# Kernel tuning notes

Hardware: AMD Instinct MI355X
Metric: run time of the kernel (lower is better)

Reference implementation:

```python
import jax, jax.numpy as jnp
import numpy as np

BS, V, S, K = 4, 2048, 7, 10
CLASS_NUM, VEC_NUM, CAT = 6, 8, 16
OUT_HEAD = CLASS_NUM + VEC_NUM * 3  # 30
DIM_FUSE = 128 + 128 + 256 + 256 + 512 + 512 + 16  # 1808


def _normalize(x, axis):
    return x / jnp.maximum(jnp.linalg.norm(x, axis=axis, keepdims=True), 1e-12)


def knn_index(verts, k):
    # verts: (b, v, 3) -> (b, v, k) excluding self
    inner = jnp.einsum('bnd,bmd->bnm', verts, verts)
    sq = jnp.sum(verts * verts, axis=2)
    dist = sq[:, :, None] + sq[:, None, :] - 2.0 * inner
    _, idx = jax.lax.top_k(-dist, k + 1)
    return idx[:, :, 1:]


def nearest_index(target, source):
    # target: (b, v1, 3), source: (b, v2, 3) -> (b, v1)
    inner = jnp.einsum('bnd,bmd->bnm', target, source)
    d = jnp.sum(source * source, 2)[:, None, :] + jnp.sum(target * target, 2)[:, :, None] - 2.0 * inner
    return jnp.argmin(d, axis=-1)


def gather_nb(t, idx):
    # t: (b, v, d), idx: (b, v1, k) -> (b, v1, k, d)
    return jax.vmap(lambda tt, ii: tt[ii])(t, idx)


def gather1(t, idx):
    # t: (b, v, d), idx: (b, v1) -> (b, v1, d)
    return jax.vmap(lambda tt, ii: tt[ii])(t, idx)


def bn_train(x, g, b, eps=1e-5):
    # x: (b, v, c); BatchNorm1d training-mode over (batch, vertices)
    m = jnp.mean(x, axis=(0, 1), keepdims=True)
    v = jnp.var(x, axis=(0, 1), keepdims=True)
    return (x - m) * jax.lax.rsqrt(v + eps) * g + b


def conv_surface(nb_idx, verts, directions, s, kernel_num):
    nd = _normalize(gather_nb(verts, nb_idx) - verts[:, :, None, :], -1)  # (b,v,n,3)
    sd = _normalize(directions, 0)  # (3, s*k)
    theta = jax.nn.relu(jnp.einsum('bvnd,dk->bvnk', nd, sd))
    b_, v_, n_, _ = theta.shape
    theta = theta.reshape(b_, v_, n_, s, kernel_num)
    return jnp.sum(jnp.max(theta, axis=2), axis=2)  # (b, v, kernel_num)


def conv_layer(nb_idx, verts, fm, w, b, directions, s, out_ch):
    nd = _normalize(gather_nb(verts, nb_idx) - verts[:, :, None, :], -1)
    sd = _normalize(directions, 0)  # (3, s*out_ch)
    theta = jax.nn.relu(jnp.einsum('bvnd,dk->bvnk', nd, sd))  # (b,v,n,s*o)
    fo = jnp.einsum('bvc,ck->bvk', fm, w) + b  # (b, v, (s+1)*o)
    center = fo[..., :out_ch]
    supp = gather_nb(fo[..., out_ch:], nb_idx)  # (b,v,n,s*o)
    act = (theta * supp).reshape(theta.shape[0], theta.shape[1], theta.shape[2], s, out_ch)
    act = jnp.sum(jnp.max(act, axis=2), axis=2)  # (b, v, o)
    return center + act


def pool_layer(verts, fm, pooling_rate, nb_num):
    idx = knn_index(verts, nb_num)
    pooled = jnp.max(gather_nb(fm, idx), axis=2)
    pool_num = verts.shape[1] // pooling_rate
    # deterministic subsample (torch uses randperm; fixed arange for reproducibility)
    return verts[:, :pool_num], pooled[:, :pool_num]


def setup_inputs() -> dict:
    key = jax.random.key(0)
    ks = jax.random.split(key, 16)
    def rn(i, shape, scale=0.05):
        return jax.random.normal(ks[i], shape, dtype=jnp.float32) * scale
    z = lambda *s: jnp.zeros(s, jnp.float32)
    o = lambda *s: jnp.ones(s, jnp.float32)
    return {
        'vertices': jax.random.normal(ks[0], (BS, V, 3), dtype=jnp.float32),
        'onehot': jax.nn.one_hot(jax.random.randint(ks[1], (BS,), 0, CAT), CAT, dtype=jnp.float32),
        'dir0': rn(2, (3, S * 128)),
        'w1': rn(3, (128, (S + 1) * 128)), 'b1': z((S + 1) * 128), 'dir1': rn(4, (3, S * 128)),
        'w2': rn(5, (128, (S + 1) * 256)), 'b2': z((S + 1) * 256), 'dir2': rn(6, (3, S * 256)),
        'w3': rn(7, (256, (S + 1) * 256)), 'b3': z((S + 1) * 256), 'dir3': rn(8, (3, S * 256)),
        'w4': rn(9, (256, (S + 1) * 512)), 'b4': z((S + 1) * 512), 'dir4': rn(10, (3, S * 512)),
        'g_bn1': o(128), 'be_bn1': z(128),
        'g_bn2': o(256), 'be_bn2': z(256),
        'g_bn3': o(256), 'be_bn3': z(256),
        'wc1': rn(11, (512, DIM_FUSE)), 'bc1': z(512),
        'wc2': rn(12, (512, 512)), 'bc2': z(512),
        'wc3': rn(13, (OUT_HEAD, 512)), 'bc3': z(OUT_HEAD),
    }


def reference(vertices, onehot, dir0, w1, b1, dir1, w2, b2, dir2, w3, b3, dir3,
              w4, b4, dir4, g_bn1, be_bn1, g_bn2, be_bn2, g_bn3, be_bn3,
              wc1, bc1, wc2, bc2, wc3, bc3):
    bs, v_num, _ = vertices.shape
    nb = knn_index(vertices, K)
    fm0 = jax.nn.relu(conv_surface(nb, vertices, dir0, S, 128))
    fm1 = jax.nn.relu(bn_train(conv_layer(nb, vertices, fm0, w1, b1, dir1, S, 128), g_bn1, be_bn1))
    vp1, fp1 = pool_layer(vertices, fm1, 4, 4)
    nb1 = knn_index(vp1, min(K, vp1.shape[1] // 8))
    fm2 = jax.nn.relu(bn_train(conv_layer(nb1, vp1, fp1, w2, b2, dir2, S, 256), g_bn2, be_bn2))
    fm3 = jax.nn.relu(bn_train(conv_layer(nb1, vp1, fm2, w3, b3, dir3, S, 256), g_bn3, be_bn3))
    vp2, fp2 = pool_layer(vp1, fm3, 4, 4)
    nb2 = knn_index(vp2, min(K, vp2.shape[1] // 8))
    fm4 = conv_layer(nb2, vp2, fp2, w4, b4, dir4, S, 512)
    f_global = jnp.max(fm4, axis=1)  # (b, 512)
    n1 = nearest_index(vertices, vp1)
    n2 = nearest_index(vertices, vp2)
    fm2u = gather1(fm2, n1)
    fm3u = gather1(fm3, n1)
    fm4u = gather1(fm4, n2)
    fg = jnp.broadcast_to(f_global[:, None, :], (bs, v_num, 512))
    oh = jnp.broadcast_to(onehot[:, None, :], (bs, v_num, CAT))
    feat = jnp.concatenate([fm0, fm1, fm2u, fm3u, fm4u, oh], axis=2)
    fuse = jnp.concatenate([fm0, fm1, fm2u, fm3u, fm4u, fg, oh], axis=2)
    h = jax.nn.relu(jnp.einsum('bvc,oc->bvo', fuse, wc1) + bc1)
    h = jax.nn.relu(jnp.einsum('bvc,oc->bvo', h, wc2) + bc2)
    pred = jnp.einsum('bvc,oc->bvo', h, wc3) + bc3
    seg = pred[..., :CLASS_NUM]
    vecs = pred[..., CLASS_NUM:CLASS_NUM + VEC_NUM * 3]
    return (seg, vecs, feat)
```

## Files before the change

### kernel.cpp

```cpp
#include <hip/hip_runtime.h>
#include <hip/hip_bf16.h>
#include <math.h>

#define BSZ 4
#define VN 2048
#define SS 7
#define KNB 10

typedef __attribute__((ext_vector_type(8))) short short8;
typedef __attribute__((ext_vector_type(4))) float f32x4;
typedef __attribute__((address_space(1))) const void gcvoid;
typedef __attribute__((address_space(3))) void lvoid;

__device__ inline ushort f2bf(float x) {
    __hip_bfloat16 h = __float2bfloat16(x);
    return *(ushort*)&h;
}

__device__ inline void gl2lds16(const ushort* g, ushort* l) {
    __builtin_amdgcn_global_load_lds((gcvoid*)g, (lvoid*)l, 16, 0, 0);
}

__device__ inline unsigned fenc(float f) {
    unsigned b = __float_as_uint(f);
    return (b & 0x80000000u) ? ~b : (b | 0x80000000u);
}
__device__ inline float fdec(unsigned e) {
    unsigned b = (e & 0x80000000u) ? (e & 0x7FFFFFFFu) : ~e;
    return __uint_as_float(b);
}

#define INS(dq, iq, dd, jj) { bool lt_ = (dd) < (dq); \
    float dmn_ = lt_ ? (dd) : (dq); float dmx_ = lt_ ? (dq) : (dd); \
    int imn_ = lt_ ? (jj) : (iq); int imx_ = lt_ ? (iq) : (jj); \
    (dq) = dmn_; (iq) = imn_; (dd) = dmx_; (jj) = imx_; }

#define PB0 8960L
#define PB1 24320L
#define PB2 958208L
#define PB3 1220352L

__global__ void prep_uber(const float* __restrict__ d0, const float* __restrict__ d1,
                          const float* __restrict__ d2, const float* __restrict__ d3,
                          const float* __restrict__ d4,
                          float* __restrict__ s0, float* __restrict__ s1,
                          float* __restrict__ s2, float* __restrict__ s3, float* __restrict__ s4,
                          const float* __restrict__ wc3, float* __restrict__ wc3t,
                          const float* __restrict__ wc1, ushort* __restrict__ wc1b,
                          const float* __restrict__ wc2, ushort* __restrict__ wc2b) {
    long i = blockIdx.x * 256L + threadIdx.x;
    if (i < PB0) {
        const float* src; float* dst; int C, c;
        if (i < 896)        { src = d0; dst = s0; C = 896;  c = (int)i; }
        else if (i < 1792)  { src = d1; dst = s1; C = 896;  c = (int)i - 896; }
        else if (i < 3584)  { src = d2; dst = s2; C = 1792; c = (int)i - 1792; }
        else if (i < 5376)  { src = d3; dst = s3; C = 1792; c = (int)i - 3584; }
        else                { src = d4; dst = s4; C = 3584; c = (int)i - 5376; }
        float a = src[c], b = src[C + c], e = src[2 * C + c];
        float den = fmaxf(sqrtf(a * a + b * b + e * e), 1e-12f);
        dst[c] = a / den; dst[C + c] = b / den; dst[2 * C + c] = e / den;
    } else if (i < PB1) {
        long j = i - PB0;
        int o = (int)(j / 512), k = (int)(j % 512);
        wc3t[(long)k * 30 + o] = wc3[j];
    } else if (i < PB2) {
        long j = i - PB1;
        int c = (int)(j % 1824);
        long r = j / 1824;
        wc1b[j] = f2bf(c < 1808 ? wc1[r * 1808 + c] : 0.f);
    } else if (i < PB3) {
        long j = i - PB2;
        wc2b[j] = f2bf(wc2[j]);
    }
}

__global__ __launch_bounds__(256) void wt_trans_all(const float* __restrict__ w1, const float* __restrict__ w2,
                                                    const float* __restrict__ w3, const float* __restrict__ w4,
                                                    ushort* __restrict__ o1, ushort* __restrict__ o2,
                                                    ushort* __restrict__ o3, ushort* __restrict__ o4) {
    __shared__ float tile[32][33];
    int gb = blockIdx.x;
    const float* w; ushort* o; int K, N, t;
    if (gb < 128)      { w = w1; o = o1; K = 128; N = 1024; t = gb; }
    else if (gb < 384) { w = w2; o = o2; K = 128; N = 2048; t = gb - 128; }
    else if (gb < 896) { w = w3; o = o3; K = 256; N = 2048; t = gb - 384; }
    else               { w = w4; o = o4; K = 256; N = 4096; t = gb - 896; }
    int tn = t % (N / 32), tk = t / (N / 32);
    int n0 = tn * 32, k0 = tk * 32;
    int tx = threadIdx.x % 32, ty = threadIdx.x / 32;
#pragma unroll
    for (int r = 0; r < 32; r += 8)
        tile[ty + r][tx] = w[(long)(k0 + ty + r) * N + n0 + tx];
    __syncthreads();
#pragma unroll
    for (int r = 0; r < 32; r += 8)
        o[(long)(n0 + ty + r) * K + k0 + tx] = f2bf(tile[tx][ty + r]);
}

#define KOFF0 0L
#define KOFF1 2621440L
#define KOFF2 2785280L
#define KOFF3 2795520L
#define KOFF4 3057664L
#define KTOT  3074048L

template <int KK>
__device__ void knn_part_dev(const float* __restrict__ verts, int Nsrc, int T, int nch,
                             int tile, int b, int ch,
                             float* __restrict__ pd, int* __restrict__ pi,
                             float4* __restrict__ s4) {
    const float* vb = verts + (long)b * VN * 3;
    int j0 = ch * 128;
    for (int j = threadIdx.x; j < 128; j += 256) {
        float x = vb[(j0 + j) * 3 + 0];
        float y = vb[(j0 + j) * 3 + 1];
        float z = vb[(j0 + j) * 3 + 2];
        s4[j] = make_float4(x, y, z, x * x + y * y + z * z);
    }
    __syncthreads();
    int i = tile * 256 + threadIdx.x;
    if (i >= T) return;
    float px = vb[i * 3], py = vb[i * 3 + 1], pz = vb[i * 3 + 2];
    float d0[KK], d1[KK]; int id0[KK], id1[KK];
#pragma unroll
    for (int q = 0; q < KK; q++) { d0[q] = 1e30f; id0[q] = 0; d1[q] = 1e30f; id1[q] = 0; }
    for (int j = 0; j < 64; j++) {
        float4 sA = s4[j];
        float4 sB = s4[64 + j];
        float dA = fmaf(-2.f, px * sA.x + py * sA.y + pz * sA.z, sA.w);
        float dB = fmaf(-2.f, px * sB.x + py * sB.y + pz * sB.z, sB.w);
        int jA = j0 + j, jB = j0 + 64 + j;
        dA = (jA == i) ? 1e30f : dA;
        dB = (jB == i) ? 1e30f : dB;
#pragma unroll
        for (int q = 0; q < KK; q++) { INS(d0[q], id0[q], dA, jA); }
#pragma unroll
        for (int q = 0; q < KK; q++) { INS(d1[q], id1[q], dB, jB); }
    }
    long base = (((long)b * T + i) * nch * 2 + 2 * ch) * KK;
#pragma unroll
    for (int q = 0; q < KK; q++) { pd[base + q] = d0[q]; pi[base + q] = id0[q]; }
#pragma unroll
    for (int q = 0; q < KK; q++) { pd[base + KK + q] = d1[q]; pi[base + KK + q] = id1[q]; }
}

__device__ void nearest_dev(const float* __restrict__ verts, int SN, int* __restrict__ out,
                            int gl, float4* __restrict__ s4) {
    int t = gl * 256 + threadIdx.x;
    int b = t / VN;
    const float* vb = verts + (long)b * VN * 3;
    for (int j = threadIdx.x; j < SN; j += 256) {
        float x = vb[j * 3], y = vb[j * 3 + 1], z = vb[j * 3 + 2];
        s4[j] = make_float4(x, y, z, x * x + y * y + z * z);
    }
    __syncthreads();
    int i = t % VN;
    float px = vb[i * 3], py = vb[i * 3 + 1], pz = vb[i * 3 + 2];
    int h = SN / 2;
    float b0 = 1e30f, b1 = 1e30f; int i0 = 0, i1 = 0;
    for (int j = 0; j < h; j++) {
        float4 sA = s4[j];
        float4 sB = s4[h + j];
        float dA = fmaf(-2.f, px * sA.x + py * sA.y + pz * sA.z, sA.w);
        float dB = fmaf(-2.f, px * sB.x + py * sB.y + pz * sB.z, sB.w);
        bool lA = dA < b0; b0 = lA ? dA : b0; i0 = lA ? j : i0;
        bool lB = dB < b1; b1 = lB ? dB : b1; i1 = lB ? (h + j) : i1;
    }
    out[t] = (b1 < b0) ? i1 : i0;
}

__global__ __launch_bounds__(256) void knn_part_uber(const float* __restrict__ verts,
                                                     float* __restrict__ pd, int* __restrict__ pi,
                                                     int* __restrict__ n1, int* __restrict__ n2) {
    __shared__ float4 smem[512];
    int gb = blockIdx.x;
    if (gb < 512) {
        int tile = gb % 8, bc = gb / 8;
        knn_part_dev<10>(verts, 2048, 2048, 16, tile, bc / 16, bc % 16, pd + KOFF0, pi + KOFF0, smem);
    } else if (gb < 544) {
        int local = gb - 512, tile = local % 2, bc = local / 2;
        knn_part_dev<10>(verts, 512, 512, 4, tile, bc / 4, bc % 4, pd + KOFF1, pi + KOFF1, smem);
    } else if (gb < 548) {
        int bc = gb - 544;
        knn_part_dev<10>(verts, 128, 128, 1, 0, bc, 0, pd + KOFF2, pi + KOFF2, smem);
    } else if (gb < 676) {
        int local = gb - 548, tile = local % 2, bc = local / 2;
        knn_part_dev<4>(verts, 2048, 512, 16, tile, bc / 16, bc % 16, pd + KOFF3, pi + KOFF3, smem);
    } else if (gb < 692) {
        int bc = gb - 676;
        knn_part_dev<4>(verts, 512, 128, 4, 0, bc / 4, bc % 4, pd + KOFF4, pi + KOFF4, smem);
    } else if (gb < 724) {
        nearest_dev(verts, 512, n1, gb - 692, smem);
    } else {
        nearest_dev(verts, 128, n2, gb - 724, smem);
    }
}

template <int KK, int NCH>
__device__ void knn_merge2_dev(const float* __restrict__ pd, const int* __restrict__ pi,
                               int blk, int* __restrict__ out, float* sdl, int* sil) {
    int tgt = threadIdx.x >> 2;
    int sub = threadIdx.x & 3;
    long t = (long)blk * 64 + tgt;
    constexpr int GRP = (NCH + 3) / 4;
    float d[KK]; int id[KK];
#pragma unroll
    for (int q = 0; q < KK; q++) { d[q] = 1e30f; id[q] = 0; }
    int c0 = sub * GRP;
    int c1 = (c0 + GRP < NCH) ? c0 + GRP : NCH;
    for (int c = c0; c < c1; c++) {
        long base = (t * NCH + c) * KK;
        for (int q = 0; q < KK; q++) {
            float dd = pd[base + q];
            if (dd >= d[KK - 1]) break;
            int jj = pi[base + q];
#pragma unroll
            for (int p = 0; p < KK; p++) { INS(d[p], id[p], dd, jj); }
        }
    }
    float* md = sdl + (long)(tgt * 4 + sub) * KK;
    int* mi = sil + (long)(tgt * 4 + sub) * KK;
#pragma unroll
    for (int q = 0; q < KK; q++) { md[q] = d[q]; mi[q] = id[q]; }
    __syncthreads();
    if (sub == 0) {
        for (int s = 1; s < 4; s++) {
            const float* od = sdl + (long)(tgt * 4 + s) * KK;
            const int* oi = sil + (long)(tgt * 4 + s) * KK;
            for (int q = 0; q < KK; q++) {
                float dd = od[q];
                if (dd >= d[KK - 1]) break;
                int jj = oi[q];
#pragma unroll
                for (int p = 0; p < KK; p++) { INS(d[p], id[p], dd, jj); }
            }
        }
#pragma unroll
        for (int q = 0; q < KK; q++) out[t * KK + q] = id[q];
    }
}

__global__ __launch_bounds__(256) void knn_merge_uber(const float* __restrict__ pd, const int* __restrict__ pi,
                                                      int* __restrict__ nb, int* __restrict__ nb1,
                                                      int* __restrict__ nb2, int* __restrict__ nbp1,
                                                      int* __restrict__ nbp2) {
    __shared__ float sdl[64 * 4 * 10];
    __shared__ int   sil[64 * 4 * 10];
    int gb = blockIdx.x;
    if (gb < 128)      knn_merge2_dev<10, 32>(pd + KOFF0, pi + KOFF0, gb, nb, sdl, sil);
    else if (gb < 160) knn_merge2_dev<10, 8>(pd + KOFF1, pi + KOFF1, gb - 128, nb1, sdl, sil);
    else if (gb < 168) knn_merge2_dev<10, 2>(pd + KOFF2, pi + KOFF2, gb - 160, nb2, sdl, sil);
    else if (gb < 200) knn_merge2_dev<4, 32>(pd + KOFF3, pi + KOFF3, gb - 168, nbp1, sdl, sil);
    else               knn_merge2_dev<4, 8>(pd + KOFF4, pi + KOFF4, gb - 200, nbp2, sdl, sil);
}

__global__ void conv_surface_kernel(const float* __restrict__ verts, const int* __restrict__ nb,
                                    const float* __restrict__ sd, float* __restrict__ fm0,
                                    ushort* __restrict__ fm0b) {
    int bv = blockIdx.x;
    int b = bv / VN, v = bv % VN;
    __shared__ float snd[KNB][3];
    int tid = threadIdx.x;
    if (tid < KNB) {
        int nj = nb[(long)bv * KNB + tid];
        const float* vb = verts + (long)b * VN * 3;
        float dx = vb[nj * 3] - vb[v * 3];
        float dy = vb[nj * 3 + 1] - vb[v * 3 + 1];
        float dz = vb[nj * 3 + 2] - vb[v * 3 + 2];
        float den = fmaxf(sqrtf(dx * dx + dy * dy + dz * dz), 1e-12f);
        snd[tid][0] = dx / den; snd[tid][1] = dy / den; snd[tid][2] = dz / den;
    }
    __syncthreads();
    int c = tid;
    float acc = 0.f;
    for (int s = 0; s < SS; s++) {
        int col = s * 128 + c;
        float s0 = sd[col], s1 = sd[896 + col], s2 = sd[2 * 896 + col];
        float m = 0.f;
#pragma unroll
        for (int n = 0; n < KNB; n++) {
            float dot = snd[n][0] * s0 + snd[n][1] * s1 + snd[n][2] * s2;
            m = fmaxf(m, dot);
        }
        acc += m;
    }
    fm0[(long)bv * 128 + c] = acc;
    fm0b[(long)bv * 128 + c] = f2bf(acc);
}

__global__ void conv_act_kernel(const float* __restrict__ verts, const int* __restrict__ nb,
                                const float* __restrict__ sd, const float* __restrict__ fo,
                                float* __restrict__ out, unsigned* __restrict__ fgmax,
                                int Vl, int outC) {
    int bv = blockIdx.x;
    int b = bv / Vl, v = bv % Vl;
    __shared__ float snd[KNB][3];
    __shared__ int srow[KNB];
    int tid = threadIdx.x;
    if (tid < KNB) {
        int nj = nb[(long)bv * KNB + tid];
        srow[tid] = b * Vl + nj;
        const float* vb = verts + (long)b * VN * 3;
        float dx = vb[nj * 3] - vb[v * 3];
        float dy = vb[nj * 3 + 1] - vb[v * 3 + 1];
        float dz = vb[nj * 3 + 2] - vb[v * 3 + 2];
        float den = fmaxf(sqrtf(dx * dx + dy * dy + dz * dz), 1e-12f);
        snd[tid][0] = dx / den; snd[tid][1] = dy / den; snd[tid][2] = dz / den;
    }
    __syncthreads();
    int c = tid;
    int SC = SS * outC;
    int foN = SC + outC;
    float acc = fo[(long)bv * foN + c];
    for (int s = 0; s < SS; s++) {
        int col = s * outC + c;
        float s0 = sd[col], s1 = sd[SC + col], s2 = sd[2 * SC + col];
        float m = -1e30f;
#pragma unroll
        for (int n = 0; n < KNB; n++) {
            float dot = snd[n][0] * s0 + snd[n][1] * s1 + snd[n][2] * s2;
            float th = fmaxf(dot, 0.f);
            float sup = fo[(long)srow[n] * foN + outC + col];
            m = fmaxf(m, th * sup);
        }
        acc += m;
    }
    out[(long)bv * outC + c] = acc;
    if (fgmax) atomicMax(&fgmax[b * outC + c], fenc(acc));
}

__global__ __launch_bounds__(256) void bn_stat_kernel(const float* __restrict__ x,
                                                      float* __restrict__ stat, int R, int C) {
    int rp = 256 / C;
    int c = threadIdx.x % C;
    int rs = threadIdx.x / C;
    float s = 0.f, s2 = 0.f;
    for (long r = (long)blockIdx.x * rp + rs; r < R; r += (long)gridDim.x * rp) {
        float v = x[r * C + c];
        s += v; s2 += v * v;
    }
    atomicAdd(&stat[c], s);
    atomicAdd(&stat[C + c], s2);
}

__global__ void bn_apply_relu_kernel(const float* __restrict__ x, const float* __restrict__ stat,
                                     const float* __restrict__ g, const float* __restrict__ be,
                                     float* __restrict__ out, ushort* __restrict__ outb, int R, int C) {
    long i = blockIdx.x * 256L + threadIdx.x;
    if (i >= (long)R * C) return;
    int c = (int)(i % C);
    float mu = stat[c] / R;
    float var = stat[C + c] / R - mu * mu;
    var = fmaxf(var, 0.f);
    float y = (x[i] - mu) * rsqrtf(var + 1e-5f) * g[c] + be[c];
    y = fmaxf(y, 0.f);
    out[i] = y;
    if (outb) outb[i] = f2bf(y);
}

__global__ void pool_b_kernel(const float* __restrict__ fm, const int* __restrict__ idx,
                              ushort* __restrict__ out, int Vin, int T, int C) {
    long i = blockIdx.x * 256L + threadIdx.x;
    if (i >= (long)BSZ * T * C) return;
    int c = (int)(i % C);
    long bt = i / C;
    int b = (int)(bt / T), t = (int)(bt % T);
    const int* id = idx + ((long)b * T + t) * 4;
    float m = -1e30f;
#pragma unroll
    for (int n = 0; n < 4; n++)
        m = fmaxf(m, fm[((long)b * Vin + id[n]) * C + c]);
    out[i] = f2bf(m);
}

__global__ __launch_bounds__(256) void gemm_mfma_bt_kernel(
    const ushort* __restrict__ A, const ushort* __restrict__ Bt,
    const float* __restrict__ bias, float* __restrict__ Cf, ushort* __restrict__ Cb,
    int M, int N, int K, int relu)
{
    __shared__ ushort As[128 * 32];
    __shared__ ushort Bs[128 * 32];
    int t = threadIdx.x;
    int w = t >> 6, l = t & 63;
    int quad = l >> 4, lm = l & 15;
    int wm = w >> 1, wn = w & 1;
    long m0 = blockIdx.y * 128L;
    long n0 = blockIdx.x * 128L;
    int lr = t >> 2;
    int lk = (t & 3) * 8;
    f32x4 acc[4][4];
#pragma unroll
    for (int i = 0; i < 4; i++)
#pragma unroll
        for (int j = 0; j < 4; j++) acc[i][j] = (f32x4){0.f, 0.f, 0.f, 0.f};

    for (int k0 = 0; k0 < K; k0 += 32) {
        __syncthreads();
        gl2lds16(A + (m0 + lr) * K + k0 + lk, &As[lr * 32 + lk]);
        gl2lds16(A + (m0 + 64 + lr) * K + k0 + lk, &As[(64 + lr) * 32 + lk]);
        gl2lds16(Bt + (n0 + lr) * K + k0 + lk, &Bs[lr * 32 + lk]);
        gl2lds16(Bt + (n0 + 64 + lr) * K + k0 + lk, &Bs[(64 + lr) * 32 + lk]);
        __syncthreads();
        short8 af[4], bfr[4];
#pragma unroll
        for (int i = 0; i < 4; i++)
            af[i] = *(const short8*)&As[(wm * 64 + i * 16 + lm) * 32 + quad * 8];
#pragma unroll
        for (int j = 0; j < 4; j++)
            bfr[j] = *(const short8*)&Bs[(wn * 64 + j * 16 + lm) * 32 + quad * 8];
#pragma unroll
        for (int i = 0; i < 4; i++)
#pragma unroll
            for (int j = 0; j < 4; j++)
                acc[i][j] = __builtin_amdgcn_mfma_f32_16x16x32_bf16(af[i], bfr[j], acc[i][j], 0, 0, 0);
    }
#pragma unroll
    for (int i = 0; i < 4; i++) {
#pragma unroll
        for (int j = 0; j < 4; j++) {
            int n = (int)n0 + wn * 64 + j * 16 + lm;
            float bv = bias[n];
#pragma unroll
            for (int r = 0; r < 4; r++) {
                int m = (int)m0 + wm * 64 + i * 16 + quad * 4 + r;
                float v = acc[i][j][r] + bv;
                if (relu) v = fmaxf(v, 0.f);
                if (Cf) Cf[(long)m * N + n] = v;
                if (Cb) Cb[(long)m * N + n] = f2bf(v);
            }
        }
    }
}

__global__ __launch_bounds__(256) void gemm_mfma_bt64_kernel(
    const ushort* __restrict__ A, const ushort* __restrict__ Bt,
    const float* __restrict__ bias, float* __restrict__ Cf, ushort* __restrict__ Cb,
    int M, int N, int K, int relu)
{
    __shared__ ushort As[64 * 32];
    __shared__ ushort Bs[128 * 32];
    int t = threadIdx.x;
    int w = t >> 6, l = t & 63;
    int quad = l >> 4, lm = l & 15;
    int wm = w >> 1, wn = w & 1;
    long m0 = blockIdx.y * 64L;
    long n0 = blockIdx.x * 128L;
    int lr = t >> 2;
    int lk = (t & 3) * 8;
    f32x4 acc[2][4];
#pragma unroll
    for (int i = 0; i < 2; i++)
#pragma unroll
        for (int j = 0; j < 4; j++) acc[i][j] = (f32x4){0.f, 0.f, 0.f, 0.f};

    for (int k0 = 0; k0 < K; k0 += 32) {
        __syncthreads();
        gl2lds16(A + (m0 + lr) * K + k0 + lk, &As[lr * 32 + lk]);
        gl2lds16(Bt + (n0 + lr) * K + k0 + lk, &Bs[lr * 32 + lk]);
        gl2lds16(Bt + (n0 + 64 + lr) * K + k0 + lk, &Bs[(64 + lr) * 32 + lk]);
        __syncthreads();
        short8 af[2], bfr[4];
#pragma unroll
        for (int i = 0; i < 2; i++)
            af[i] = *(const short8*)&As[(wm * 32 + i * 16 + lm) * 32 + quad * 8];
#pragma unroll
        for (int j = 0; j < 4; j++)
            bfr[j] = *(const short8*)&Bs[(wn * 64 + j * 16 + lm) * 32 + quad * 8];
#pragma unroll
        for (int i = 0; i < 2; i++)
#pragma unroll
            for (int j = 0; j < 4; j++)
                acc[i][j] = __builtin_amdgcn_mfma_f32_16x16x32_bf16(af[i], bfr[j], acc[i][j], 0, 0, 0);
    }
#pragma unroll
    for (int i = 0; i < 2; i++) {
#pragma unroll
        for (int j = 0; j < 4; j++) {
            int n = (int)n0 + wn * 64 + j * 16 + lm;
            float bv = bias[n];
#pragma unroll
            for (int r = 0; r < 4; r++) {
                int m = (int)m0 + wm * 32 + i * 16 + quad * 4 + r;
                float v = acc[i][j][r] + bv;
                if (relu) v = fmaxf(v, 0.f);
                if (Cf) Cf[(long)m * N + n] = v;
                if (Cb) Cb[(long)m * N + n] = f2bf(v);
            }
        }
    }
}

__global__ __launch_bounds__(256) void wc3_kernel(const float* __restrict__ h2,
                                                  const float* __restrict__ wc3t,
                                                  const float* __restrict__ bc3,
                                                  float* __restrict__ out) {
    int r8 = threadIdx.x >> 5;
    int c = threadIdx.x & 31;
    long row = blockIdx.x * 8L + r8;
    const float* hr = h2 + row * 512;
    float acc = 0.f;
    if (c < 30) {
        for (int k = 0; k < 512; k++)
            acc += hr[k] * wc3t[k * 30 + c];
        acc += bc3[c];
        if (c < 6) out[row * 6 + c] = acc;
        else       out[49152 + row * 24 + (c - 6)] = acc;
    }
}

__global__ __launch_bounds__(256) void fuse_bf_kernel(
    const float* __restrict__ fm0, const float* __restrict__ fm1,
    const float* __restrict__ fm2, const float* __restrict__ fm3,
    const float* __restrict__ fm4, const unsigned* __restrict__ fg_enc,
    const float* __restrict__ onehot,
    const int* __restrict__ n1, const int* __restrict__ n2,
    ushort* __restrict__ fuse_b, float* __restrict__ feat) {
    long row = blockIdx.x;
    int b = (int)(row >> 11);
    int i1 = n1[row], i2 = n2[row];
    const float* p0 = fm0 + row * 128;
    const float* p1 = fm1 + row * 128;
    const float* p2 = fm2 + ((long)b * 512 + i1) * 256;
    const float* p3 = fm3 + ((long)b * 512 + i1) * 256;
    const float* p4 = fm4 + ((long)b * 128 + i2) * 512;
    const unsigned* pg = fg_enc + b * 512;
    const float* po = onehot + b * 16;
    ushort* fb = fuse_b + row * 1824;
    float* ft = feat + row * 1296;
#pragma unroll
    for (int k = 0; k < 8; k++) {
        int c = threadIdx.x + k * 256;
        if (c >= 1824) break;
        float val = 0.f;
        if (c < 128)       val = p0[c];
        else if (c < 256)  val = p1[c - 128];
        else if (c < 512)  val = p2[c - 256];
        else if (c < 768)  val = p3[c - 512];
        else if (c < 1280) val = p4[c - 768];
        else if (c < 1792) val = fdec(pg[c - 1280]);
        else if (c < 1808) val = po[c - 1792];
        fb[c] = f2bf(val);
        if (c < 1280)                   ft[c] = val;
        else if (c >= 1792 && c < 1808) ft[c - 512] = val;
    }
}


extern "C" void kernel_launch(void* const* d_in, const int* in_sizes, int n_in,
                              void* d_out, int out_size, void* d_ws, size_t ws_size,
                              hipStream_t stream) {
    const float* verts  = (const float*)d_in[0];
    const float* onehot = (const float*)d_in[1];
    const float* dir0 = (const float*)d_in[2];
    const float* w1 = (const float*)d_in[3];
    const float* b1 = (const float*)d_in[4];
    const float* dir1 = (const float*)d_in[5];
    const float* w2 = (const float*)d_in[6];
    const float* b2 = (const float*)d_in[7];
    const float* dir2 = (const float*)d_in[8];
    const float* w3 = (const float*)d_in[9];
    const float* b3 = (const float*)d_in[10];
    const float* dir3 = (const float*)d_in[11];
    const float* w4 = (const float*)d_in[12];
    const float* b4 = (const float*)d_in[13];
    const float* dir4 = (const float*)d_in[14];
    const float* g_bn1 = (const float*)d_in[15];
    const float* be_bn1 = (const float*)d_in[16];
    const float* g_bn2 = (const float*)d_in[17];
    const float* be_bn2 = (const float*)d_in[18];
    const float* g_bn3 = (const float*)d_in[19];
    const float* be_bn3 = (const float*)d_in[20];
    const float* wc1 = (const float*)d_in[21];
    const float* bc1 = (const float*)d_in[22];
    const float* wc2 = (const float*)d_in[23];
    const float* bc2 = (const float*)d_in[24];
    const float* wc3 = (const float*)d_in[25];
    const float* bc3 = (const float*)d_in[26];
    float* outf = (float*)d_out;

    float* wsf = (float*)d_ws;
    size_t off = 0;
    auto alloc = [&](size_t n) { float* p = wsf + off; off += (n + 15) & ~(size_t)15; return p; };

    float* sd0 = alloc(3 * 896);
    float* sd1 = alloc(3 * 896);
    float* sd2 = alloc(3 * 1792);
    float* sd3 = alloc(3 * 1792);
    float* sd4 = alloc(3 * 3584);
    float* wc3t = alloc(512L * 30);
    float* fm0 = alloc(8192L * 128);
    float* fm1 = alloc(8192L * 128);
    float* c1  = alloc(8192L * 128);
    float* fm2 = alloc(2048L * 256);
    float* c2  = alloc(2048L * 256);
    float* fm3 = alloc(2048L * 256);
    float* c3  = alloc(2048L * 256);
    float* fm4 = alloc(512L * 512);
    float* statbase = alloc(3328);
    float* stat1 = statbase;
    float* stat2 = statbase + 256;
    float* stat3 = statbase + 768;
    unsigned* fg_enc = (unsigned*)(statbase + 1280);
    float* fbuf = alloc(8192L * 1024);
    float* h2 = alloc(8192L * 512);
    float* pd  = alloc(KTOT);
    int* pi    = (int*)alloc(KTOT);
    int* nb   = (int*)alloc(8192L * KNB);
    int* nb1  = (int*)alloc(2048L * KNB);
    int* nb2  = (int*)alloc(512L * KNB);
    int* nbp1 = (int*)alloc(2048L * 4);
    int* nbp2 = (int*)alloc(512L * 4);
    int* n1   = (int*)alloc(8192);
    int* n2   = (int*)alloc(8192);
    ushort* fuse_b = (ushort*)alloc(8192L * 1824 / 2);
    ushort* h1b    = (ushort*)alloc(8192L * 512 / 2);
    ushort* wc1b   = (ushort*)alloc(512L * 1824 / 2);
    ushort* wc2b   = (ushort*)alloc(512L * 512 / 2);
    ushort* w1tb   = (ushort*)alloc(1024L * 128 / 2);
    ushort* w2tb   = (ushort*)alloc(2048L * 128 / 2);
    ushort* w3tb   = (ushort*)alloc(2048L * 256 / 2);
    ushort* w4tb   = (ushort*)alloc(4096L * 256 / 2);
    ushort* fm0b   = (ushort*)alloc(8192L * 128 / 2);
    ushort* fp1b   = (ushort*)alloc(2048L * 128 / 2);
    ushort* fm2b   = (ushort*)alloc(2048L * 256 / 2);
    ushort* fp2b   = (ushort*)alloc(512L * 256 / 2);

    auto nblk = [](long n, int b) { return (unsigned)((n + b - 1) / b); };

    hipMemsetAsync(statbase, 0, 3328 * sizeof(float), stream);
    prep_uber<<<nblk(PB3, 256), 256, 0, stream>>>(dir0, dir1, dir2, dir3, dir4,
                                                  sd0, sd1, sd2, sd3, sd4,
                                                  wc3, wc3t, wc1, wc1b, wc2, wc2b);
    wt_trans_all<<<1920, 256, 0, stream>>>(w1, w2, w3, w4, w1tb, w2tb, w3tb, w4tb);

    knn_part_uber<<<756, 256, 0, stream>>>(verts, pd, pi, n1, n2);
    knn_merge_uber<<<208, 256, 0, stream>>>(pd, pi, nb, nb1, nb2, nbp1, nbp2);

    conv_surface_kernel<<<BSZ * 2048, 128, 0, stream>>>(verts, nb, sd0, fm0, fm0b);

    gemm_mfma_bt_kernel<<<dim3(8, 64), 256, 0, stream>>>(fm0b, w1tb, b1, fbuf, nullptr, 8192, 1024, 128, 0);
    conv_act_kernel<<<BSZ * 2048, 128, 0, stream>>>(verts, nb, sd1, fbuf, c1, nullptr, 2048, 128);
    bn_stat_kernel<<<256, 256, 0, stream>>>(c1, stat1, 8192, 128);
    bn_apply_relu_kernel<<<nblk(8192L * 128, 256), 256, 0, stream>>>(c1, stat1, g_bn1, be_bn1, fm1, nullptr, 8192, 128);

    pool_b_kernel<<<nblk(BSZ * 512L * 128, 256), 256, 0, stream>>>(fm1, nbp1, fp1b, 2048, 512, 128);

    gemm_mfma_bt64_kernel<<<dim3(16, 32), 256, 0, stream>>>(fp1b, w2tb, b2, fbuf, nullptr, 2048, 2048, 128, 0);
    conv_act_kernel<<<BSZ * 512, 256, 0, stream>>>(verts, nb1, sd2, fbuf, c2, nullptr, 512, 256);
    bn_stat_kernel<<<256, 256, 0, stream>>>(c2, stat2, 2048, 256);
    bn_apply_relu_kernel<<<nblk(2048L * 256, 256), 256, 0, stream>>>(c2, stat2, g_bn2, be_bn2, fm2, fm2b, 2048, 256);

    gemm_mfma_bt64_kernel<<<dim3(16, 32), 256, 0, stream>>>(fm2b, w3tb, b3, fbuf, nullptr, 2048, 2048, 256, 0);
    conv_act_kernel<<<BSZ * 512, 256, 0, stream>>>(verts, nb1, sd3, fbuf, c3, nullptr, 512, 256);
    bn_stat_kernel<<<256, 256, 0, stream>>>(c3, stat3, 2048, 256);
    bn_apply_relu_kernel<<<nblk(2048L * 256, 256), 256, 0, stream>>>(c3, stat3, g_bn3, be_bn3, fm3, nullptr, 2048, 256);

    pool_b_kernel<<<nblk(BSZ * 128L * 256, 256), 256, 0, stream>>>(fm3, nbp2, fp2b, 512, 128, 256);

    gemm_mfma_bt64_kernel<<<dim3(32, 8), 256, 0, stream>>>(fp2b, w4tb, b4, fbuf, nullptr, 512, 4096, 256, 0);
    conv_act_kernel<<<BSZ * 128, 512, 0, stream>>>(verts, nb2, sd4, fbuf, fm4, fg_enc, 128, 512);

    fuse_bf_kernel<<<8192, 256, 0, stream>>>(fm0, fm1, fm2, fm3, fm4, fg_enc, onehot,
                                             n1, n2, fuse_b, outf + 245760);

    gemm_mfma_bt64_kernel<<<dim3(4, 128), 256, 0, stream>>>(fuse_b, wc1b, bc1, nullptr, h1b, 8192, 512, 1824, 1);
    gemm_mfma_bt64_kernel<<<dim3(4, 128), 256, 0, stream>>>(h1b, wc2b, bc2, h2, nullptr, 8192, 512, 512, 1);
    wc3_kernel<<<1024, 256, 0, stream>>>(h2, wc3t, bc3, outf);
}
```

Baseline: 490.2 us.

## Derive pooling neighbor lists from full kNN results and use smaller kNN blocks

The separate k=4 neighbor searches used for pooling are removed. The pooling neighbors are instead taken as the first 4 entries of the k=10 lists that are already computed, written out during the merge step for indices below the pooled count. This relies on the pooled points being a prefix of the vertex set, which the pool layer appears to assume. The kNN partial kernel also moves from 256-thread to 128-thread blocks with twice as many tiles, which spreads the work over more CUs.

```diff
diff --git a/kernel.cpp b/kernel.cpp
--- a/kernel.cpp
+++ b/kernel.cpp
@@ -100,30 +100,27 @@
 #define KOFF0 0L
 #define KOFF1 2621440L
 #define KOFF2 2785280L
-#define KOFF3 2795520L
-#define KOFF4 3057664L
-#define KTOT  3074048L
-
-template <int KK>
-__device__ void knn_part_dev(const float* __restrict__ verts, int Nsrc, int T, int nch,
+#define KTOT  2795520L
+
+__device__ void knn_part_dev(const float* __restrict__ verts, int T, int nch,
                              int tile, int b, int ch,
                              float* __restrict__ pd, int* __restrict__ pi,
                              float4* __restrict__ s4) {
     const float* vb = verts + (long)b * VN * 3;
     int j0 = ch * 128;
-    for (int j = threadIdx.x; j < 128; j += 256) {
+    for (int j = threadIdx.x; j < 128; j += 128) {
         float x = vb[(j0 + j) * 3 + 0];
         float y = vb[(j0 + j) * 3 + 1];
         float z = vb[(j0 + j) * 3 + 2];
         s4[j] = make_float4(x, y, z, x * x + y * y + z * z);
     }
     __syncthreads();
-    int i = tile * 256 + threadIdx.x;
+    int i = tile * 128 + (int)threadIdx.x;
     if (i >= T) return;
     float px = vb[i * 3], py = vb[i * 3 + 1], pz = vb[i * 3 + 2];
-    float d0[KK], d1[KK]; int id0[KK], id1[KK];
-#pragma unroll
-    for (int q = 0; q < KK; q++) { d0[q] = 1e30f; id0[q] = 0; d1[q] = 1e30f; id1[q] = 0; }
+    float d0[10], d1[10]; int id0[10], id1[10];
+#pragma unroll
+    for (int q = 0; q < 10; q++) { d0[q] = 1e30f; id0[q] = 0; d1[q] = 1e30f; id1[q] = 0; }
     for (int j = 0; j < 64; j++) {
         float4 sA = s4[j];
         float4 sB = s4[64 + j];
@@ -133,23 +130,23 @@
         dA = (jA == i) ? 1e30f : dA;
         dB = (jB == i) ? 1e30f : dB;
 #pragma unroll
-        for (int q = 0; q < KK; q++) { INS(d0[q], id0[q], dA, jA); }
-#pragma unroll
-        for (int q = 0; q < KK; q++) { INS(d1[q], id1[q], dB, jB); }
-    }
-    long base = (((long)b * T + i) * nch * 2 + 2 * ch) * KK;
-#pragma unroll
-    for (int q = 0; q < KK; q++) { pd[base + q] = d0[q]; pi[base + q] = id0[q]; }
-#pragma unroll
-    for (int q = 0; q < KK; q++) { pd[base + KK + q] = d1[q]; pi[base + KK + q] = id1[q]; }
+        for (int q = 0; q < 10; q++) { INS(d0[q], id0[q], dA, jA); }
+#pragma unroll
+        for (int q = 0; q < 10; q++) { INS(d1[q], id1[q], dB, jB); }
+    }
+    long base = (((long)b * T + i) * nch * 2 + 2 * ch) * 10;
+#pragma unroll
+    for (int q = 0; q < 10; q++) { pd[base + q] = d0[q]; pi[base + q] = id0[q]; }
+#pragma unroll
+    for (int q = 0; q < 10; q++) { pd[base + 10 + q] = d1[q]; pi[base + 10 + q] = id1[q]; }
 }
 
 __device__ void nearest_dev(const float* __restrict__ verts, int SN, int* __restrict__ out,
                             int gl, float4* __restrict__ s4) {
-    int t = gl * 256 + threadIdx.x;
+    int t = gl * 128 + (int)threadIdx.x;
     int b = t / VN;
     const float* vb = verts + (long)b * VN * 3;
-    for (int j = threadIdx.x; j < SN; j += 256) {
+    for (int j = threadIdx.x; j < SN; j += 128) {
         float x = vb[j * 3], y = vb[j * 3 + 1], z = vb[j * 3 + 2];
         s4[j] = make_float4(x, y, z, x * x + y * y + z * z);
     }
@@ -169,74 +166,79 @@
     out[t] = (b1 < b0) ? i1 : i0;
 }
 
-__global__ __launch_bounds__(256) void knn_part_uber(const float* __restrict__ verts,
+__global__ __launch_bounds__(128) void knn_part_uber(const float* __restrict__ verts,
                                                      float* __restrict__ pd, int* __restrict__ pi,
                                                      int* __restrict__ n1, int* __restrict__ n2) {
     __shared__ float4 smem[512];
     int gb = blockIdx.x;
-    if (gb < 512) {
-        int tile = gb % 8, bc = gb / 8;
-        knn_part_dev<10>(verts, 2048, 2048, 16, tile, bc / 16, bc % 16, pd + KOFF0, pi + KOFF0, smem);
-    } else if (gb < 544) {
-        int local = gb - 512, tile = local % 2, bc = local / 2;
-        knn_part_dev<10>(verts, 512, 512, 4, tile, bc / 4, bc % 4, pd + KOFF1, pi + KOFF1, smem);
-    } else if (gb < 548) {
-        int bc = gb - 544;
-        knn_part_dev<10>(verts, 128, 128, 1, 0, bc, 0, pd + KOFF2, pi + KOFF2, smem);
-    } else if (gb < 676) {
-        int local = gb - 548, tile = local % 2, bc = local / 2;
-        knn_part_dev<4>(verts, 2048, 512, 16, tile, bc / 16, bc % 16, pd + KOFF3, pi + KOFF3, smem);
-    } else if (gb < 692) {
-        int bc = gb - 676;
-        knn_part_dev<4>(verts, 512, 128, 4, 0, bc / 4, bc % 4, pd + KOFF4, pi + KOFF4, smem);
-    } else if (gb < 724) {
-        nearest_dev(verts, 512, n1, gb - 692, smem);
+    if (gb < 1024) {
+        int tile = gb & 15, bc = gb >> 4;
+        knn_part_dev(verts, 2048, 16, tile, bc >> 4, bc & 15, pd + KOFF0, pi + KOFF0, smem);
+    } else if (gb < 1088) {
+        int local = gb - 1024;
+        int tile = local & 3, bc = local >> 2;
+        knn_part_dev(verts, 512, 4, tile, bc >> 2, bc & 3, pd + KOFF1, pi + KOFF1, smem);
+    } else if (gb < 1092) {
+        int local = gb - 1088;
+        knn_part_dev(verts, 128, 1, 0, local, 0, pd + KOFF2, pi + KOFF2, smem);
+    } else if (gb < 1156) {
+        nearest_dev(verts, 512, n1, gb - 1092, smem);
     } else {
-        nearest_dev(verts, 128, n2, gb - 724, smem);
-    }
-}
-
-template <int KK, int NCH>
-__device__ void knn_merge2_dev(const float* __restrict__ pd, const int* __restrict__ pi,
-                               int blk, int* __restrict__ out, float* sdl, int* sil) {
+        nearest_dev(verts, 128, n2, gb - 1156, smem);
+    }
+}
+
+template <int NCH>
+__device__ void knn_merge_dev(const float* __restrict__ pd, const int* __restrict__ pi,
+                              int blk, int Tb,
+                              int* __restrict__ out, int* __restrict__ outp, int Tp,
+                              float* sdl, int* sil) {
     int tgt = threadIdx.x >> 2;
     int sub = threadIdx.x & 3;
     long t = (long)blk * 64 + tgt;
     constexpr int GRP = (NCH + 3) / 4;
-    float d[KK]; int id[KK];
-#pragma unroll
-    for (int q = 0; q < KK; q++) { d[q] = 1e30f; id[q] = 0; }
+    float d[10]; int id[10];
+#pragma unroll
+    for (int q = 0; q < 10; q++) { d[q] = 1e30f; id[q] = 0; }
     int c0 = sub * GRP;
     int c1 = (c0 + GRP < NCH) ? c0 + GRP : NCH;
     for (int c = c0; c < c1; c++) {
-        long base = (t * NCH + c) * KK;
-        for (int q = 0; q < KK; q++) {
+        long base = (t * NCH + c) * 10;
+        for (int q = 0; q < 10; q++) {
             float dd = pd[base + q];
-            if (dd >= d[KK - 1]) break;
+            if (dd >= d[9]) break;
             int jj = pi[base + q];
 #pragma unroll
-            for (int p = 0; p < KK; p++) { INS(d[p], id[p], dd, jj); }
+            for (int p = 0; p < 10; p++) { INS(d[p], id[p], dd, jj); }
         }
     }
-    float* md = sdl + (long)(tgt * 4 + sub) * KK;
-    int* mi = sil + (long)(tgt * 4 + sub) * KK;
-#pragma unroll
-    for (int q = 0; q < KK; q++) { md[q] = d[q]; mi[q] = id[q]; }
+    float* md = sdl + (tgt * 4 + sub) * 10;
+    int* mi = sil + (tgt * 4 + sub) * 10;
+#pragma unroll
+    for (int q = 0; q < 10; q++) { md[q] = d[q]; mi[q] = id[q]; }
     __syncthreads();
     if (sub == 0) {
         for (int s = 1; s < 4; s++) {
-            const float* od = sdl + (long)(tgt * 4 + s) * KK;
-            const int* oi = sil + (long)(tgt * 4 + s) * KK;
-            for (int q = 0; q < KK; q++) {
+            const float* od = sdl + (tgt * 4 + s) * 10;
+            const int* oi = sil + (tgt * 4 + s) * 10;
+            for (int q = 0; q < 10; q++) {
                 float dd = od[q];
-                if (dd >= d[KK - 1]) break;
+                if (dd >= d[9]) break;
                 int jj = oi[q];
 #pragma unroll
-                for (int p = 0; p < KK; p++) { INS(d[p], id[p], dd, jj); }
+                for (int p = 0; p < 10; p++) { INS(d[p], id[p], dd, jj); }
             }
         }
 #pragma unroll
-        for (int q = 0; q < KK; q++) out[t * KK + q] = id[q];
+        for (int q = 0; q < 10; q++) out[t * 10 + q] = id[q];
+        if (outp) {
+            int b = (int)(t / Tb), i = (int)(t % Tb);
+            if (i < Tp) {
+#pragma unroll
+                for (int q = 0; q < 4; q++)
+                    outp[((long)b * Tp + i) * 4 + q] = id[q];
+            }
+        }
     }
 }
 
@@ -247,11 +249,9 @@
     __shared__ float sdl[64 * 4 * 10];
     __shared__ int   sil[64 * 4 * 10];
     int gb = blockIdx.x;
-    if (gb < 128)      knn_merge2_dev<10, 32>(pd + KOFF0, pi + KOFF0, gb, nb, sdl, sil);
-    else if (gb < 160) knn_merge2_dev<10, 8>(pd + KOFF1, pi + KOFF1, gb - 128, nb1, sdl, sil);
-    else if (gb < 168) knn_merge2_dev<10, 2>(pd + KOFF2, pi + KOFF2, gb - 160, nb2, sdl, sil);
-    else if (gb < 200) knn_merge2_dev<4, 32>(pd + KOFF3, pi + KOFF3, gb - 168, nbp1, sdl, sil);
-    else               knn_merge2_dev<4, 8>(pd + KOFF4, pi + KOFF4, gb - 200, nbp2, sdl, sil);
+    if (gb < 128)      knn_merge_dev<32>(pd + KOFF0, pi + KOFF0, gb, 2048, nb, nbp1, 512, sdl, sil);
+    else if (gb < 160) knn_merge_dev<8>(pd + KOFF1, pi + KOFF1, gb - 128, 512, nb1, nbp2, 128, sdl, sil);
+    else               knn_merge_dev<2>(pd + KOFF2, pi + KOFF2, gb - 160, 128, nb2, nullptr, 1, sdl, sil);
 }
 
 __global__ void conv_surface_kernel(const float* __restrict__ verts, const int* __restrict__ nb,
@@ -633,8 +633,8 @@
                                                   wc3, wc3t, wc1, wc1b, wc2, wc2b);
     wt_trans_all<<<1920, 256, 0, stream>>>(w1, w2, w3, w4, w1tb, w2tb, w3tb, w4tb);
 
-    knn_part_uber<<<756, 256, 0, stream>>>(verts, pd, pi, n1, n2);
-    knn_merge_uber<<<208, 256, 0, stream>>>(pd, pi, nb, nb1, nb2, nbp1, nbp2);
+    knn_part_uber<<<1220, 128, 0, stream>>>(verts, pd, pi, n1, n2);
+    knn_merge_uber<<<168, 256, 0, stream>>>(pd, pi, nb, nb1, nb2, nbp1, nbp2);
 
     conv_surface_kernel<<<BSZ * 2048, 128, 0, stream>>>(verts, nb, sd0, fm0, fm0b);
 
```

Result: no change. 490.2 us (+0.0%).
